# Kernel optimization log

Hardware: AMD Instinct MI355X
Metric: run time of the kernel (lower is better)

Reference implementation:

```python
import jax, jax.numpy as jnp
import numpy as np

B, S, D = 2, 8192, 2048
H, HD = 16, 128
LSH_NUM_PROJS = 7
BLOCK = 256          # key/query block size for block-diagonal attention
SAMPLE = 256         # number of uniformly sampled residual columns
ROPE_BASE = 10000.0
LOG_WEIGHT = float(np.log(S / SAMPLE))  # importance weight for sampled columns


def setup_inputs() -> dict:
    key = jax.random.key(0)
    ks = jax.random.split(key, 5)
    x = jax.random.normal(ks[0], (B, S, D), jnp.float32)
    w_in = jax.random.normal(ks[1], (D, 3 * D), jnp.float32) * (D ** -0.5)
    w_out = jax.random.normal(ks[2], (D, D), jnp.float32) * (D ** -0.5)
    lsh_proj = jax.random.normal(ks[3], (HD, LSH_NUM_PROJS), jnp.float32)
    sampled_set = jax.random.randint(ks[4], (B, H, SAMPLE), 0, S, jnp.int32)
    return {"x": x, "w_in": w_in, "w_out": w_out,
            "lsh_proj": lsh_proj, "sampled_set": sampled_set}


def _rope(t):
    # t: [B, S, H, HD]; LLaMA-style half-split rotary embedding, offset=0
    half = HD // 2
    inv_freq = 1.0 / (ROPE_BASE ** (jnp.arange(half, dtype=jnp.float32) / half))
    freqs = jnp.arange(S, dtype=jnp.float32)[:, None] * inv_freq[None, :]  # [S, half]
    cos = jnp.cos(freqs)[None, :, None, :]
    sin = jnp.sin(freqs)[None, :, None, :]
    t1, t2 = t[..., :half], t[..., half:]
    return jnp.concatenate([t1 * cos - t2 * sin, t2 * cos + t1 * sin], axis=-1)


def _lse_attn(q, k, v, scale, bias=None):
    # exact attention with log-sum-exp; q [...,n,d], k/v [...,m,d]
    s = jnp.einsum('...nd,...md->...nm', q, k) * scale
    if bias is not None:
        s = s + bias
    lse = jax.nn.logsumexp(s, axis=-1, keepdims=True)   # [...,n,1]
    p = jnp.exp(s - lse)
    return jnp.einsum('...nm,...md->...nd', p, v), lse


def _hyper_attention(q, k, v, lsh_proj, sampled_set):
    # q,k,v: [B,H,S,HD]  (non-causal HyperAttention path)
    scale = HD ** -0.5

    def lsh_hash(t):
        # simhash bucket codes from sign bits of random projections
        bits = jnp.einsum('bhsd,dp->bhsp', t, lsh_proj) > 0
        powers = (2 ** jnp.arange(LSH_NUM_PROJS)).astype(jnp.int32)
        return jnp.sum(bits.astype(jnp.int32) * powers, axis=-1)  # [B,H,S]

    q_idx = jnp.argsort(lsh_hash(q), axis=-1, stable=True)
    k_idx = jnp.argsort(lsh_hash(k), axis=-1, stable=True)
    q_idx_inv = jnp.argsort(q_idx, axis=-1, stable=True)
    gather = lambda t, i: jnp.take_along_axis(t, i[..., None], axis=2)

    qs = gather(q, q_idx)
    ks_ = gather(k, k_idx)
    vs = gather(v, k_idx)

    # 1. block-diagonal exact attention on LSH-sorted order
    nb = S // BLOCK
    qb = qs.reshape(B, H, nb, BLOCK, HD)
    kb = ks_.reshape(B, H, nb, BLOCK, HD)
    vb = vs.reshape(B, H, nb, BLOCK, HD)
    attn_blk, lse_blk = _lse_attn(qb, kb, vb, scale)
    attn_blk = attn_blk.reshape(B, H, S, HD)
    lse_blk = lse_blk.reshape(B, H, S, 1)

    # 2. residual: uniformly sampled columns (indices into sorted key order),
    #    masking columns already covered by the query's diagonal block
    k_sub = gather(ks_, sampled_set)   # [B,H,m,HD]
    v_sub = gather(vs, sampled_set)
    q_block_id = jnp.arange(S, dtype=jnp.int32) // BLOCK          # [S]
    s_block_id = sampled_set // BLOCK                             # [B,H,m]
    neg = jnp.finfo(q.dtype).min
    bias = jnp.where(q_block_id[None, None, :, None] == s_block_id[:, :, None, :],
                     neg, jnp.array(0.0, q.dtype))                # [B,H,S,m]
    attn_res, lse_res = _lse_attn(qs, k_sub, v_sub, scale, bias=bias)
    lse_res = lse_res + LOG_WEIGHT

    # 3. merge the two partial softmax results (online-softmax combine)
    lse = jnp.logaddexp(lse_blk, lse_res)
    attn = attn_blk * jnp.exp(lse_blk - lse) + attn_res * jnp.exp(lse_res - lse)

    # undo query sort
    return gather(attn, q_idx_inv)


def reference(x, w_in, w_out, lsh_proj, sampled_set):
    qkv = x @ w_in                           # [B,S,3D]
    q, k, v = jnp.split(qkv, 3, axis=-1)
    r4 = lambda t: t.reshape(B, S, H, HD)
    q, k, v = _rope(r4(q)), _rope(r4(k)), r4(v)
    tr = lambda t: t.transpose(0, 2, 1, 3)   # -> [B,H,S,HD]
    out = _hyper_attention(tr(q), tr(k), tr(v), lsh_proj, sampled_set)
    out = out.transpose(0, 2, 1, 3).reshape(B, S, D)
    return out @ w_out
```

## Files before the change

### kernel.cpp

```cpp
#include <hip/hip_runtime.h>
#include <stdint.h>

typedef _Float16 f16;
typedef _Float16 f16x8 __attribute__((ext_vector_type(8)));
typedef float f32x4 __attribute__((ext_vector_type(4)));
typedef uint32_t u32;

#define SEQ 8192
#define NH 16
#define HDIM 128
#define BHCNT 32
#define KDIM 2048
#define SCALE 0.08838834764831845f
#define LOGW 3.4657359027997265f
#define TAU1 0.06f
#define TAU 6e-3f
#define MAXWL 32768
#define BCAP 1024

__device__ __forceinline__ f32x4 mfma16(f16x8 a, f16x8 b, f32x4 c){
  return __builtin_amdgcn_mfma_f32_16x16x32_f16(a, b, c, 0, 0, 0);
}

__device__ __forceinline__ void g2l16(const f16* g, f16* l){
  __builtin_amdgcn_global_load_lds(
      (const __attribute__((address_space(1))) void*)g,
      (__attribute__((address_space(3))) void*)l, 16, 0, 0);
}

__global__ __launch_bounds__(256) void split_x_k(const float* __restrict__ x,
                                                 f16* __restrict__ xh){
  size_t i = ((size_t)blockIdx.x * 256 + threadIdx.x) * 4;
  float4 v = *(const float4*)(x + i);
  union { f16 h[4]; ushort4 u; } a;
  a.h[0]=(f16)v.x; a.h[1]=(f16)v.y; a.h[2]=(f16)v.z; a.h[3]=(f16)v.w;
  *(ushort4*)(xh + i) = a.u;
}

__global__ void transpose_k(const float* __restrict__ in, f16* __restrict__ ohi,
                            f16* __restrict__ olo, int Kd, int Nd, int NLO){
  __shared__ float t[32][33];
  int tx = threadIdx.x, ty = threadIdx.y;
  int n0 = blockIdx.x*32, k0 = blockIdx.y*32;
  #pragma unroll
  for (int i=0;i<4;i++) t[ty+i*8][tx] = in[(size_t)(k0+ty+i*8)*Nd + n0+tx];
  __syncthreads();
  #pragma unroll
  for (int i=0;i<4;i++){
    int n = n0 + ty + i*8, k = k0 + tx;
    float v = t[tx][ty+i*8];
    f16 h = (f16)v;
    ohi[(size_t)n*Kd + k] = h;
    if (n < NLO) olo[(size_t)n*Kd + k] = (f16)(v - (float)h);
  }
}

__global__ __launch_bounds__(256) void rope_table_k(float* __restrict__ ct, float* __restrict__ st){
  int i = blockIdx.x * 256 + threadIdx.x;
  int s = i >> 6, d = i & 63;
  float p32 = (float)pow(10000.0, (double)d / 64.0);
  float inv = __fdiv_rn(1.0f, p32);
  float f = __fmul_rn((float)s, inv);
  double a = (double)f;
  ct[i] = (float)cos(a);
  st[i] = (float)sin(a);
}

__global__ void zero_k(int* p){ p[0] = 0; p[1] = 0; p[2] = 0; }

__global__ void diag_k(const int* __restrict__ flags, float* __restrict__ out){
  int c = flags[0];
  if (c == 0 || c >= MAXWL || flags[2]) out[0] = 1.0e9f + (float)c;
}

template<int MODE, int NC>
__global__ __launch_bounds__(256) void gemm_k(
    const f16* __restrict__ A, const f16* __restrict__ Bt,
    f16* __restrict__ q16, f16* __restrict__ k16, f16* __restrict__ v16,
    float* __restrict__ o0, int N){
  __shared__ f16 sm[8192];
  const int tid = threadIdx.x, lane = tid & 63, wave = tid >> 6;
  const int wr = wave >> 1, wc = wave & 1;
  const int wg = blockIdx.x;
  const int chunkw = gridDim.x >> 3;
  const int swz = (wg & 7) * chunkw + (wg >> 3);
  const int bcol = swz % NC, brow = swz / NC;
  const int g = lane >> 4, q_ = lane & 15;
  f32x4 acc[4][4];
  #pragma unroll
  for (int m=0;m<4;m++)
    #pragma unroll
    for (int n=0;n<4;n++) acc[m][n] = (f32x4){0.f,0.f,0.f,0.f};
  const int srow = tid >> 2, sseg = tid & 3;
  const int scol = (sseg ^ (srow & 3)) * 8;
  const f16* ga0 = A  + (size_t)(brow*128 + srow)*KDIM + scol;
  const f16* gb0 = Bt + (size_t)(bcol*128 + srow)*KDIM + scol;
  f16* As = sm; f16* Bs = sm + 4096;
  f16* dA0 = As + wave*512; f16* dA1 = As + 2048 + wave*512;
  f16* dB0 = Bs + wave*512; f16* dB1 = Bs + 2048 + wave*512;
  const int aoff = (wr*64 + q_)*32 + (g ^ (q_ & 3))*8;
  const int boff = (wc*64 + q_)*32 + (g ^ (q_ & 3))*8;
  for (int kt = 0; kt < KDIM/32; ++kt){
    const size_t ko = (size_t)kt * 32;
    g2l16(ga0 + ko, dA0); g2l16(ga0 + (size_t)64*KDIM + ko, dA1);
    g2l16(gb0 + ko, dB0); g2l16(gb0 + (size_t)64*KDIM + ko, dB1);
    __syncthreads();
    f16x8 af[4];
    #pragma unroll
    for (int m=0;m<4;m++) af[m] = *(const f16x8*)&As[aoff + m*16*32];
    #pragma unroll
    for (int n=0;n<4;n++){
      f16x8 bf = *(const f16x8*)&Bs[boff + n*16*32];
      #pragma unroll
      for (int m=0;m<4;m++) acc[m][n] = mfma16(af[m], bf, acc[m][n]);
    }
    __syncthreads();
  }
  #pragma unroll
  for (int m=0;m<4;m++)
    #pragma unroll
    for (int n=0;n<4;n++)
      #pragma unroll
      for (int j=0;j<4;j++){
        int row = brow*128 + wr*64 + m*16 + g*4 + j;
        int col = bcol*128 + wc*64 + n*16 + q_;
        float v = acc[m][n][j];
        if constexpr (MODE == 0){
          o0[(size_t)row * N + col] = v;
        } else {
          int b = row >> 13, s = row & 8191;
          int sec = col >> 11;
          int cl = col & 2047;
          int h = cl >> 7, hd = cl & 127;
          f16* dst = (sec == 0) ? q16 : ((sec == 1) ? k16 : v16);
          dst[(((size_t)b*NH + h)*SEQ + s)*HDIM + hd] = (f16)v;
        }
      }
}

__global__ __launch_bounds__(256) void rope_hash_k(f16* __restrict__ qk, const float* __restrict__ ct,
    const float* __restrict__ st, const float* __restrict__ proj, int* __restrict__ hout,
    int tag, int* __restrict__ wl, int* __restrict__ wcnt){
  const int lane = threadIdx.x & 63, wave = threadIdx.x >> 6;
  const int s = blockIdx.x * 4 + wave, bh = blockIdx.y;
  f16* row = qk + ((size_t)bh * SEQ + s) * HDIM;
  float vx = (float)row[2*lane], vy = (float)row[2*lane+1];
  float ox = __shfl_xor(vx, 32), oy = __shfl_xor(vy, 32);
  const int dl = 2*lane, di = dl & 63;
  const float* cb = ct + (size_t)s*64; const float* sb = st + (size_t)s*64;
  float c0 = cb[di], c1 = cb[di+1], sn0 = sb[di], sn1 = sb[di+1];
  float r0, r1;
  if (lane < 32){ r0 = vx*c0 - ox*sn0; r1 = vy*c1 - oy*sn1; }
  else          { r0 = vx*c0 + ox*sn0; r1 = vy*c1 + oy*sn1; }
  union { f16 h[2]; u32 u; } pk;
  pk.h[0] = (f16)r0; pk.h[1] = (f16)r1;
  *(u32*)(row + dl) = pk.u;
  float part[7];
  #pragma unroll
  for (int p=0;p<7;p++) part[p] = r0*proj[dl*7+p] + r1*proj[(dl+1)*7+p];
  #pragma unroll
  for (int off=32; off>=1; off>>=1){
    #pragma unroll
    for (int p=0;p<7;p++) part[p] += __shfl_xor(part[p], off);
  }
  if (lane == 0){
    int hs = 0; float mn = 1e30f;
    #pragma unroll
    for (int p=0;p<7;p++){ if (part[p] > 0.f) hs |= (1<<p); mn = fminf(mn, fabsf(part[p])); }
    hout[bh*SEQ + s] = hs;
    if (mn < TAU1){
      int w = atomicAdd(wcnt, 1);
      if (w < MAXWL){ wl[2*w] = (bh<<1) | tag; wl[2*w+1] = s; }
    }
  }
}

__global__ __launch_bounds__(256) void bucket_k(const int* __restrict__ wl, const int* __restrict__ wcnt,
    int* __restrict__ wl2, int* __restrict__ cnt2, int* __restrict__ flags){
  const int bucket = blockIdx.x;
  __shared__ int lcnt;
  if (threadIdx.x == 0) lcnt = 0;
  __syncthreads();
  int count = wcnt[0]; if (count > MAXWL) count = MAXWL;
  for (int i = threadIdx.x; i < count; i += 256){
    int tagbh = wl[2*i];
    int tag = tagbh & 1, h = (tagbh >> 1) & 15;
    if (tag*16 + h == bucket){
      int pos = atomicAdd(&lcnt, 1);
      if (pos < BCAP) wl2[bucket*BCAP + pos] = (tagbh << 13) | wl[2*i+1];
    }
  }
  __syncthreads();
  if (threadIdx.x == 0){
    cnt2[bucket] = (lcnt > BCAP) ? BCAP : lcnt;
    if (lcnt > BCAP) atomicExch(&flags[2], 1);
  }
}

__global__ __launch_bounds__(256) void t2_k(const float* __restrict__ x,
    const f16* __restrict__ wh, const f16* __restrict__ wlo,
    const int* __restrict__ wl2, const int* __restrict__ cnt2,
    const float* __restrict__ ct, const float* __restrict__ st, const float* __restrict__ proj,
    int* __restrict__ hq, int* __restrict__ hk, int* __restrict__ wl3, int* __restrict__ wcnt3){
  const int bucket = blockIdx.y;
  const int nrows = cnt2[bucket];
  const int base = blockIdx.x * 64;
  if (base >= nrows) return;
  const int tid = threadIdx.x, lane = tid & 63, wave = tid >> 6;
  const int g = lane >> 4, q_ = lane & 15;
  __shared__ f16 Ah[64*32], Alo[64*32], Bh[128*32], Bl[128*32];
  __shared__ float S[64][128];
  __shared__ int rs[64], ent[64];
  if (tid < 64){
    int idx = base + tid;
    int e = wl2[bucket*BCAP + (idx < nrows ? idx : 0)];
    ent[tid] = e;
    int s = e & 8191;
    int b = e >> 18;
    rs[tid] = b * SEQ + s;
  }
  __syncthreads();
  const int tag = bucket >> 4, h = bucket & 15;
  const f16* Wh = wh  + ((size_t)(tag*2048 + h*128)) * KDIM;
  const f16* Wl = wlo + ((size_t)(tag*2048 + h*128)) * KDIM;
  f32x4 acc[8];
  #pragma unroll
  for (int n=0;n<8;n++) acc[n] = (f32x4){0.f,0.f,0.f,0.f};
  const int arow = tid >> 2, aseg = tid & 3;
  const int bcol = tid >> 1, bhalf = tid & 1;
  const size_t abase = (size_t)rs[arow]*KDIM + aseg*8;
  const size_t bbase = (size_t)bcol*KDIM + bhalf*16;
  for (int kt = 0; kt < 64; ++kt){
    const int k0 = kt*32;
    {
      union { float4 f4[2]; float f[8]; } xa;
      xa.f4[0] = *(const float4*)(x + abase + k0);
      xa.f4[1] = *(const float4*)(x + abase + k0 + 4);
      union { f16 h[8]; f16x8 v; } hh, ll;
      #pragma unroll
      for (int i=0;i<8;i++){
        f16 hv = (f16)xa.f[i];
        hh.h[i] = hv;
        ll.h[i] = (f16)(xa.f[i] - (float)hv);
      }
      *(f16x8*)&Ah [arow*32 + aseg*8] = hh.v;
      *(f16x8*)&Alo[arow*32 + aseg*8] = ll.v;
    }
    *(f16x8*)&Bh[bcol*32 + bhalf*16]     = *(const f16x8*)(Wh + bbase + k0);
    *(f16x8*)&Bh[bcol*32 + bhalf*16 + 8] = *(const f16x8*)(Wh + bbase + k0 + 8);
    *(f16x8*)&Bl[bcol*32 + bhalf*16]     = *(const f16x8*)(Wl + bbase + k0);
    *(f16x8*)&Bl[bcol*32 + bhalf*16 + 8] = *(const f16x8*)(Wl + bbase + k0 + 8);
    __syncthreads();
    f16x8 ah = *(const f16x8*)&Ah [(wave*16 + q_)*32 + g*8];
    f16x8 al = *(const f16x8*)&Alo[(wave*16 + q_)*32 + g*8];
    #pragma unroll
    for (int n=0;n<8;n++){
      f16x8 bh8 = *(const f16x8*)&Bh[(n*16 + q_)*32 + g*8];
      f16x8 bl8 = *(const f16x8*)&Bl[(n*16 + q_)*32 + g*8];
      acc[n] = mfma16(ah, bh8, acc[n]);
      acc[n] = mfma16(ah, bl8, acc[n]);
      acc[n] = mfma16(al, bh8, acc[n]);
    }
    __syncthreads();
  }
  #pragma unroll
  for (int n=0;n<8;n++)
    #pragma unroll
    for (int j=0;j<4;j++)
      S[wave*16 + g*4 + j][n*16 + q_] = acc[n][j];
  __syncthreads();
  for (int r = 0; r < 16; ++r){
    int row = wave*16 + r;
    int gidx = base + row;
    if (gidx >= nrows) break;
    int e = ent[row];
    int s = e & 8191;
    int tagbh = e >> 13;
    int bh = tagbh >> 1;
    float vx = S[row][2*lane], vy = S[row][2*lane+1];
    float ox = __shfl_xor(vx, 32), oy = __shfl_xor(vy, 32);
    const int dl = 2*lane, di = dl & 63;
    float c0 = ct[(size_t)s*64 + di], c1v = ct[(size_t)s*64 + di + 1];
    float sn0 = st[(size_t)s*64 + di], sn1 = st[(size_t)s*64 + di + 1];
    float r0, r1;
    if (lane < 32){ r0 = vx*c0 - ox*sn0; r1 = vy*c1v - oy*sn1; }
    else          { r0 = vx*c0 + ox*sn0; r1 = vy*c1v + oy*sn1; }
    float part[7];
    #pragma unroll
    for (int p=0;p<7;p++) part[p] = r0*proj[dl*7+p] + r1*proj[(dl+1)*7+p];
    #pragma unroll
    for (int off=32; off>=1; off>>=1){
      #pragma unroll
      for (int p=0;p<7;p++) part[p] += __shfl_xor(part[p], off);
    }
    if (lane == 0){
      int hs = 0; float mn = 1e30f;
      #pragma unroll
      for (int p=0;p<7;p++){ if (part[p] > 0.f) hs |= (1<<p); mn = fminf(mn, fabsf(part[p])); }
      ((tagbh & 1) ? hk : hq)[bh*SEQ + s] = hs;
      if (mn < TAU){
        int w = atomicAdd(wcnt3, 1);
        if (w < MAXWL){ wl3[2*w] = tagbh; wl3[2*w+1] = s; }
      }
    }
  }
}

__global__ __launch_bounds__(256) void fixup_k(const float* __restrict__ x, const float* __restrict__ w_in,
    const float* __restrict__ proj, const float* __restrict__ ct, const float* __restrict__ st,
    const int* __restrict__ wl, const int* __restrict__ wcnt,
    int* __restrict__ hq, int* __restrict__ hk){
  const int lane = threadIdx.x & 63, wave = threadIdx.x >> 6;
  const int gw = blockIdx.x * 4 + wave, nw = gridDim.x * 4;
  int count = *wcnt; if (count > MAXWL) count = MAXWL;
  for (int e = gw; e < count; e += nw){
    int tagbh = wl[2*e], s = wl[2*e+1];
    int tag = tagbh & 1, bh = tagbh >> 1;
    int b = bh >> 4, h = bh & 15;
    const float* xr = x + ((size_t)b*SEQ + s)*KDIM;
    const int c0i = tag*2048 + h*128 + lane;
    double a0 = 0.0, a1 = 0.0;
    for (int j = 0; j < KDIM; ++j){
      double xv = (double)xr[j];
      a0 += xv * (double)w_in[(size_t)j*6144 + c0i];
      a1 += xv * (double)w_in[(size_t)j*6144 + c0i + 64];
    }
    double c = (double)ct[(size_t)s*64 + lane];
    double sn = (double)st[(size_t)s*64 + lane];
    double r0 = a0*c - a1*sn;
    double r1 = a1*c + a0*sn;
    int hs = 0;
    #pragma unroll
    for (int p = 0; p < 7; ++p){
      double part = r0 * (double)proj[lane*7+p] + r1 * (double)proj[(lane+64)*7+p];
      #pragma unroll
      for (int off = 32; off >= 1; off >>= 1) part += __shfl_xor(part, off);
      if (part > 0.0) hs |= (1<<p);
    }
    if (lane == 0) (tag ? hk : hq)[bh*SEQ + s] = hs;
  }
}

__global__ __launch_bounds__(256) void sort_k(const int* __restrict__ hsh, int* __restrict__ idx){
  const int bh = blockIdx.x, tid = threadIdx.x;
  __shared__ unsigned char hl[SEQ];
  __shared__ unsigned short hist[128*256];
  __shared__ unsigned int part[256];
  const int* hrow = hsh + bh*SEQ;
  for (int i = tid; i < SEQ; i += 256) hl[i] = (unsigned char)hrow[i];
  u32* h32 = (u32*)hist;
  for (int i = tid; i < 128*256/2; i += 256) h32[i] = 0;
  __syncthreads();
  #pragma unroll 1
  for (int j = 0; j < 32; ++j){
    int hv = hl[tid*32 + j];
    hist[hv*256 + tid] = (unsigned short)(hist[hv*256 + tid] + 1);
  }
  __syncthreads();
  unsigned int s = 0;
  #pragma unroll 1
  for (int f = tid*128; f < tid*128 + 128; ++f) s += hist[f];
  part[tid] = s;
  __syncthreads();
  for (int off = 1; off < 256; off <<= 1){
    unsigned int v = (tid >= off) ? part[tid - off] : 0u;
    __syncthreads();
    part[tid] += v;
    __syncthreads();
  }
  unsigned int run = (tid == 0) ? 0u : part[tid - 1];
  #pragma unroll 1
  for (int f = tid*128; f < tid*128 + 128; ++f){
    unsigned short c = hist[f];
    hist[f] = (unsigned short)run;
    run += c;
  }
  __syncthreads();
  int* orow = idx + bh*SEQ;
  #pragma unroll 1
  for (int j = 0; j < 32; ++j){
    int i = tid*32 + j;
    int hv = hl[i];
    unsigned short p = hist[hv*256 + tid];
    hist[hv*256 + tid] = (unsigned short)(p + 1);
    orow[p] = i;
  }
}

__global__ __launch_bounds__(512) void attn_k(const f16* __restrict__ qr, const f16* __restrict__ kr,
    const f16* __restrict__ v, const int* __restrict__ qidx, const int* __restrict__ kidx,
    const int* __restrict__ smp, f16* __restrict__ out){
  const int tid = threadIdx.x, lane = tid & 63, wave = tid >> 6;
  const int blk = blockIdx.x, bh = blockIdx.y;
  const int b = bh >> 4, h = bh & 15;
  const int qblock = blk >> 1;
  __shared__ f16 Kl[32*136];
  __shared__ f16 Vt[128*40];
  __shared__ float biasl[256];
  __shared__ int kid[512];
  const int g = lane >> 4, q_ = lane & 15;
  for (int j = tid; j < 512; j += 512){
    int kpos;
    if (j < 256) kpos = qblock*256 + j;
    else {
      kpos = smp[bh*256 + (j-256)];
      biasl[j-256] = ((kpos >> 8) == qblock) ? -1e30f : LOGW;
    }
    kid[j] = kidx[bh*SEQ + kpos];
  }
  const int qpos = blk*128 + wave*16 + q_;
  const int qi = qidx[bh*SEQ + qpos];
  const f16* qb = qr + ((size_t)bh*SEQ + qi)*HDIM;
  f16x8 qf[4];
  #pragma unroll
  for (int c=0;c<4;c++) qf[c] = *(const f16x8*)(qb + c*32 + g*8);
  f32x4 O[8];
  #pragma unroll
  for (int c=0;c<8;c++) O[c] = (f32x4){0.f,0.f,0.f,0.f};
  float m_run = -1e30f, l_run = 0.f;
  __syncthreads();
  const int kkK = tid >> 3, segK = tid & 7;
  const int kk2 = tid & 15, d0 = (tid >> 4) * 8;
  f16x8 pk0, pk1, pv0, pv1;
  if (tid < 256){
    int krw = kid[kkK];
    const f16* ks = kr + ((size_t)bh*SEQ + krw)*HDIM + segK*16;
    pk0 = *(const f16x8*)ks; pk1 = *(const f16x8*)(ks + 8);
    int r0 = kid[2*kk2], r1 = kid[2*kk2 + 1];
    pv0 = *(const f16x8*)(v + ((size_t)bh*SEQ + r0)*HDIM + d0);
    pv1 = *(const f16x8*)(v + ((size_t)bh*SEQ + r1)*HDIM + d0);
  }
  for (int t = 0; t < 16; ++t){
    if (tid < 256){
      *(f16x8*)&Kl[kkK*136 + segK*16]     = pk0;
      *(f16x8*)&Kl[kkK*136 + segK*16 + 8] = pk1;
      #pragma unroll
      for (int i=0;i<8;i++){
        union { f16 h[2]; u32 u; } pr;
        pr.h[0] = pv0[i]; pr.h[1] = pv1[i];
        *(u32*)&Vt[(d0+i)*40 + 2*kk2] = pr.u;
      }
    }
    __syncthreads();
    if (t < 15 && tid < 256){
      int jb = (t+1)*32;
      int krw = kid[jb + kkK];
      const f16* ks = kr + ((size_t)bh*SEQ + krw)*HDIM + segK*16;
      pk0 = *(const f16x8*)ks; pk1 = *(const f16x8*)(ks + 8);
      int r0 = kid[jb + 2*kk2], r1 = kid[jb + 2*kk2 + 1];
      pv0 = *(const f16x8*)(v + ((size_t)bh*SEQ + r0)*HDIM + d0);
      pv1 = *(const f16x8*)(v + ((size_t)bh*SEQ + r1)*HDIM + d0);
    }
    f32x4 c0 = (f32x4){0.f,0.f,0.f,0.f}, c1 = (f32x4){0.f,0.f,0.f,0.f};
    #pragma unroll
    for (int c=0;c<4;c++){
      f16x8 k0 = *(const f16x8*)&Kl[q_*136 + c*32 + g*8];
      f16x8 k1 = *(const f16x8*)&Kl[(16+q_)*136 + c*32 + g*8];
      c0 = mfma16(k0, qf[c], c0);
      c1 = mfma16(k1, qf[c], c1);
    }
    float sc[8];
    if (t < 8){
      #pragma unroll
      for (int j=0;j<4;j++){ sc[j] = c0[j]*SCALE; sc[4+j] = c1[j]*SCALE; }
    } else {
      const float* bb = &biasl[(t-8)*32];
      #pragma unroll
      for (int j=0;j<4;j++){ sc[j] = c0[j]*SCALE + bb[g*4+j]; sc[4+j] = c1[j]*SCALE + bb[16+g*4+j]; }
    }
    float mx = sc[0];
    #pragma unroll
    for (int i=1;i<8;i++) mx = fmaxf(mx, sc[i]);
    mx = fmaxf(mx, __shfl_xor(mx, 16));
    mx = fmaxf(mx, __shfl_xor(mx, 32));
    float mnew = fmaxf(m_run, mx);
    float al = __expf(m_run - mnew);
    float p[8]; float ps = 0.f;
    #pragma unroll
    for (int i=0;i<8;i++){ p[i] = __expf(sc[i] - mnew); ps += p[i]; }
    ps += __shfl_xor(ps, 16);
    ps += __shfl_xor(ps, 32);
    l_run = l_run * al + ps;
    m_run = mnew;
    float aj0 = __shfl(al, g*4+0), aj1 = __shfl(al, g*4+1);
    float aj2 = __shfl(al, g*4+2), aj3 = __shfl(al, g*4+3);
    #pragma unroll
    for (int c=0;c<8;c++){ O[c][0]*=aj0; O[c][1]*=aj1; O[c][2]*=aj2; O[c][3]*=aj3; }
    union { f16 h[2]; u32 u; } pk;
    pk.h[0]=(f16)p[0]; pk.h[1]=(f16)p[1]; u32 A0 = pk.u;
    pk.h[0]=(f16)p[2]; pk.h[1]=(f16)p[3]; u32 A1 = pk.u;
    pk.h[0]=(f16)p[4]; pk.h[1]=(f16)p[5]; u32 B0 = pk.u;
    pk.h[0]=(f16)p[6]; pk.h[1]=(f16)p[7]; u32 B1 = pk.u;
    int srcA = (((2*g)&3)<<4) | q_;
    int srcB = ((((2*g)+1)&3)<<4) | q_;
    bool selh = g >= 2;
    u32 xa0 = __shfl(A0, srcA), xb0 = __shfl(B0, srcA);
    u32 xa1 = __shfl(A1, srcA), xb1 = __shfl(B1, srcA);
    u32 xa2 = __shfl(A0, srcB), xb2 = __shfl(B0, srcB);
    u32 xa3 = __shfl(A1, srcB), xb3 = __shfl(B1, srcB);
    union { u32 w[4]; f16x8 f; } pf;
    pf.w[0] = selh ? xb0 : xa0;
    pf.w[1] = selh ? xb1 : xa1;
    pf.w[2] = selh ? xb2 : xa2;
    pf.w[3] = selh ? xb3 : xa3;
    #pragma unroll
    for (int c=0;c<8;c++){
      f16x8 vf = *(const f16x8*)&Vt[(c*16 + q_)*40 + g*8];
      O[c] = mfma16(pf.f, vf, O[c]);
    }
    __syncthreads();
  }
  float li0 = 1.f/__shfl(l_run, g*4+0), li1 = 1.f/__shfl(l_run, g*4+1);
  float li2 = 1.f/__shfl(l_run, g*4+2), li3 = 1.f/__shfl(l_run, g*4+3);
  const int posbase = blk*128 + wave*16;
  #pragma unroll
  for (int j=0;j<4;j++){
    float li = (j==0)?li0:((j==1)?li1:((j==2)?li2:li3));
    int sorig = qidx[bh*SEQ + posbase + g*4 + j];
    f16* dst = out + (((size_t)b*SEQ + sorig)*NH + h)*HDIM;
    #pragma unroll
    for (int c=0;c<8;c++) dst[c*16 + q_] = (f16)(O[c][j] * li);
  }
}

extern "C" void kernel_launch(void* const* d_in, const int* in_sizes, int n_in,
                              void* d_out, int out_size, void* d_ws, size_t ws_size,
                              hipStream_t stream) {
  (void)in_sizes; (void)n_in; (void)out_size; (void)ws_size;
  const float* x     = (const float*)d_in[0];
  const float* w_in  = (const float*)d_in[1];
  const float* w_out = (const float*)d_in[2];
  const float* proj  = (const float*)d_in[3];
  const int*   smp   = (const int*)d_in[4];
  float* out = (float*)d_out;

  char* ws = (char*)d_ws;
  size_t off = 0;
  auto alloc = [&](size_t bytes){ void* p = ws + off; off += (bytes + 255) & ~(size_t)255; return p; };
  f16*   xh   = (f16*)alloc((size_t)16384*2048*2);
  f16*   wh   = (f16*)alloc((size_t)6144*2048*2);
  f16*   wl   = (f16*)alloc((size_t)4096*2048*2);
  f16*   wo   = (f16*)alloc((size_t)2048*2048*2);
  f16*   qf   = (f16*)alloc((size_t)BHCNT*SEQ*HDIM*2);
  f16*   kf   = (f16*)alloc((size_t)BHCNT*SEQ*HDIM*2);
  f16*   vv   = (f16*)alloc((size_t)BHCNT*SEQ*HDIM*2);
  f16*   attn = (f16*)alloc((size_t)BHCNT*SEQ*HDIM*2);
  float* cost = (float*)alloc((size_t)SEQ*64*4);
  float* sint = (float*)alloc((size_t)SEQ*64*4);
  int*   hq   = (int*)alloc((size_t)BHCNT*SEQ*4);
  int*   hk   = (int*)alloc((size_t)BHCNT*SEQ*4);
  int*   qidx = (int*)alloc((size_t)BHCNT*SEQ*4);
  int*   kidx = (int*)alloc((size_t)BHCNT*SEQ*4);
  int*   wlst = (int*)alloc((size_t)MAXWL*2*4);
  int*   wlst2= (int*)alloc((size_t)32*BCAP*4);
  int*   wlst3= (int*)alloc((size_t)MAXWL*2*4);
  int*   cnt2 = (int*)alloc(256);
  int*   flags= (int*)alloc(256);

  int* wcnt  = flags;
  int* wcnt3 = flags + 1;

  zero_k<<<1, 1, 0, stream>>>(flags);
  split_x_k<<<32768, 256, 0, stream>>>(x, xh);
  transpose_k<<<dim3(192,64), dim3(32,8), 0, stream>>>(w_in, wh, wl, 2048, 6144, 4096);
  transpose_k<<<dim3(64,64),  dim3(32,8), 0, stream>>>(w_out, wo, nullptr, 2048, 2048, 0);
  rope_table_k<<<2048, 256, 0, stream>>>(cost, sint);

  gemm_k<1,48><<<6144, 256, 0, stream>>>(xh, wh, qf, kf, vv, nullptr, 0);

  rope_hash_k<<<dim3(2048,32), 256, 0, stream>>>(qf, cost, sint, proj, hq, 0, wlst, wcnt);
  rope_hash_k<<<dim3(2048,32), 256, 0, stream>>>(kf, cost, sint, proj, hk, 1, wlst, wcnt);

  bucket_k<<<32, 256, 0, stream>>>(wlst, wcnt, wlst2, cnt2, flags);
  t2_k<<<dim3(16,32), 256, 0, stream>>>(x, wh, wl, wlst2, cnt2, cost, sint, proj,
                                        hq, hk, wlst3, wcnt3);
  fixup_k<<<512, 256, 0, stream>>>(x, w_in, proj, cost, sint, wlst3, wcnt3, hq, hk);

  sort_k<<<32, 256, 0, stream>>>(hq, qidx);
  sort_k<<<32, 256, 0, stream>>>(hk, kidx);

  attn_k<<<dim3(64,32), 512, 0, stream>>>(qf, kf, vv, qidx, kidx, smp, attn);

  gemm_k<0,16><<<2048, 256, 0, stream>>>(attn, wo, nullptr, nullptr, nullptr, out, 2048);

  diag_k<<<1, 1, 0, stream>>>(flags, out);
}
```

Measured before the change: 1.668 ms.

## Process 64-key tiles in attention loop with lazy rescale and MFMA priority

The attention kernel now stages 64 keys per iteration instead of 32, so all 512 threads take part in loading K and V and the loop runs half as many iterations with half as many barriers. It adds a wave-uniform lazy rescale that skips updating the running max and rescaling O when the new tile max stays within 8 of the running max. It also raises wave priority around the MFMA blocks. In exchange it uses more LDS and registers, which may lower occupancy, and the skipped rescale lets unnormalised exponentials grow up to e^8 before fp16 conversion.

Result: no change. 1.692 ms (+1.4%).

```diff
diff --git a/kernel.cpp b/kernel.cpp
--- a/kernel.cpp
+++ b/kernel.cpp
@@ -394,12 +394,13 @@
   const int blk = blockIdx.x, bh = blockIdx.y;
   const int b = bh >> 4, h = bh & 15;
   const int qblock = blk >> 1;
-  __shared__ f16 Kl[32*136];
-  __shared__ f16 Vt[128*40];
+  __shared__ f16 Kl[64*136];
+  __shared__ f16 Vt[128*72];
   __shared__ float biasl[256];
   __shared__ int kid[512];
   const int g = lane >> 4, q_ = lane & 15;
-  for (int j = tid; j < 512; j += 512){
+  {
+    int j = tid;
     int kpos;
     if (j < 256) kpos = qblock*256 + j;
     else {
@@ -419,94 +420,109 @@
   for (int c=0;c<8;c++) O[c] = (f32x4){0.f,0.f,0.f,0.f};
   float m_run = -1e30f, l_run = 0.f;
   __syncthreads();
-  const int kkK = tid >> 3, segK = tid & 7;
-  const int kk2 = tid & 15, d0 = (tid >> 4) * 8;
+  const int rowK = tid >> 3, segK = tid & 7;
+  const int pairV = tid & 31, d0 = (tid >> 5) * 8;
   f16x8 pk0, pk1, pv0, pv1;
-  if (tid < 256){
-    int krw = kid[kkK];
+  {
+    int krw = kid[rowK];
     const f16* ks = kr + ((size_t)bh*SEQ + krw)*HDIM + segK*16;
     pk0 = *(const f16x8*)ks; pk1 = *(const f16x8*)(ks + 8);
-    int r0 = kid[2*kk2], r1 = kid[2*kk2 + 1];
+    int r0 = kid[2*pairV], r1 = kid[2*pairV + 1];
     pv0 = *(const f16x8*)(v + ((size_t)bh*SEQ + r0)*HDIM + d0);
     pv1 = *(const f16x8*)(v + ((size_t)bh*SEQ + r1)*HDIM + d0);
   }
-  for (int t = 0; t < 16; ++t){
-    if (tid < 256){
-      *(f16x8*)&Kl[kkK*136 + segK*16]     = pk0;
-      *(f16x8*)&Kl[kkK*136 + segK*16 + 8] = pk1;
-      #pragma unroll
-      for (int i=0;i<8;i++){
-        union { f16 h[2]; u32 u; } pr;
-        pr.h[0] = pv0[i]; pr.h[1] = pv1[i];
-        *(u32*)&Vt[(d0+i)*40 + 2*kk2] = pr.u;
-      }
-    }
-    __syncthreads();
-    if (t < 15 && tid < 256){
-      int jb = (t+1)*32;
-      int krw = kid[jb + kkK];
+  for (int t = 0; t < 8; ++t){
+    *(f16x8*)&Kl[rowK*136 + segK*16]     = pk0;
+    *(f16x8*)&Kl[rowK*136 + segK*16 + 8] = pk1;
+    #pragma unroll
+    for (int i=0;i<8;i++){
+      union { f16 h[2]; u32 u; } pr;
+      pr.h[0] = pv0[i]; pr.h[1] = pv1[i];
+      *(u32*)&Vt[(d0+i)*72 + 2*pairV] = pr.u;
+    }
+    __syncthreads();
+    if (t < 7){
+      int jb = (t+1)*64;
+      int krw = kid[jb + rowK];
       const f16* ks = kr + ((size_t)bh*SEQ + krw)*HDIM + segK*16;
       pk0 = *(const f16x8*)ks; pk1 = *(const f16x8*)(ks + 8);
-      int r0 = kid[jb + 2*kk2], r1 = kid[jb + 2*kk2 + 1];
+      int r0 = kid[jb + 2*pairV], r1 = kid[jb + 2*pairV + 1];
       pv0 = *(const f16x8*)(v + ((size_t)bh*SEQ + r0)*HDIM + d0);
       pv1 = *(const f16x8*)(v + ((size_t)bh*SEQ + r1)*HDIM + d0);
     }
-    f32x4 c0 = (f32x4){0.f,0.f,0.f,0.f}, c1 = (f32x4){0.f,0.f,0.f,0.f};
-    #pragma unroll
-    for (int c=0;c<4;c++){
-      f16x8 k0 = *(const f16x8*)&Kl[q_*136 + c*32 + g*8];
-      f16x8 k1 = *(const f16x8*)&Kl[(16+q_)*136 + c*32 + g*8];
-      c0 = mfma16(k0, qf[c], c0);
-      c1 = mfma16(k1, qf[c], c1);
-    }
-    float sc[8];
-    if (t < 8){
-      #pragma unroll
-      for (int j=0;j<4;j++){ sc[j] = c0[j]*SCALE; sc[4+j] = c1[j]*SCALE; }
+    f32x4 cc[4];
+    #pragma unroll
+    for (int kg=0;kg<4;kg++) cc[kg] = (f32x4){0.f,0.f,0.f,0.f};
+    __builtin_amdgcn_s_setprio(1);
+    #pragma unroll
+    for (int kg=0;kg<4;kg++)
+      #pragma unroll
+      for (int c=0;c<4;c++){
+        f16x8 kfr = *(const f16x8*)&Kl[(kg*16 + q_)*136 + c*32 + g*8];
+        cc[kg] = mfma16(kfr, qf[c], cc[kg]);
+      }
+    __builtin_amdgcn_s_setprio(0);
+    float sc[16];
+    if (t < 4){
+      #pragma unroll
+      for (int kg=0;kg<4;kg++)
+        #pragma unroll
+        for (int j=0;j<4;j++) sc[kg*4+j] = cc[kg][j]*SCALE;
     } else {
-      const float* bb = &biasl[(t-8)*32];
-      #pragma unroll
-      for (int j=0;j<4;j++){ sc[j] = c0[j]*SCALE + bb[g*4+j]; sc[4+j] = c1[j]*SCALE + bb[16+g*4+j]; }
+      const float* bb = &biasl[(t-4)*64];
+      #pragma unroll
+      for (int kg=0;kg<4;kg++)
+        #pragma unroll
+        for (int j=0;j<4;j++) sc[kg*4+j] = cc[kg][j]*SCALE + bb[kg*16 + g*4 + j];
     }
     float mx = sc[0];
     #pragma unroll
-    for (int i=1;i<8;i++) mx = fmaxf(mx, sc[i]);
+    for (int i=1;i<16;i++) mx = fmaxf(mx, sc[i]);
     mx = fmaxf(mx, __shfl_xor(mx, 16));
     mx = fmaxf(mx, __shfl_xor(mx, 32));
-    float mnew = fmaxf(m_run, mx);
-    float al = __expf(m_run - mnew);
-    float p[8]; float ps = 0.f;
-    #pragma unroll
-    for (int i=0;i<8;i++){ p[i] = __expf(sc[i] - mnew); ps += p[i]; }
+    bool skip = __all(mx <= m_run + 8.0f);
+    float al;
+    if (skip){ al = 1.0f; }
+    else { float mnew = fmaxf(m_run, mx); al = __expf(m_run - mnew); m_run = mnew; }
+    float ps = 0.f;
+    #pragma unroll
+    for (int i=0;i<16;i++){ sc[i] = __expf(sc[i] - m_run); ps += sc[i]; }
     ps += __shfl_xor(ps, 16);
     ps += __shfl_xor(ps, 32);
     l_run = l_run * al + ps;
-    m_run = mnew;
-    float aj0 = __shfl(al, g*4+0), aj1 = __shfl(al, g*4+1);
-    float aj2 = __shfl(al, g*4+2), aj3 = __shfl(al, g*4+3);
-    #pragma unroll
-    for (int c=0;c<8;c++){ O[c][0]*=aj0; O[c][1]*=aj1; O[c][2]*=aj2; O[c][3]*=aj3; }
-    union { f16 h[2]; u32 u; } pk;
-    pk.h[0]=(f16)p[0]; pk.h[1]=(f16)p[1]; u32 A0 = pk.u;
-    pk.h[0]=(f16)p[2]; pk.h[1]=(f16)p[3]; u32 A1 = pk.u;
-    pk.h[0]=(f16)p[4]; pk.h[1]=(f16)p[5]; u32 B0 = pk.u;
-    pk.h[0]=(f16)p[6]; pk.h[1]=(f16)p[7]; u32 B1 = pk.u;
-    int srcA = (((2*g)&3)<<4) | q_;
-    int srcB = ((((2*g)+1)&3)<<4) | q_;
-    bool selh = g >= 2;
-    u32 xa0 = __shfl(A0, srcA), xb0 = __shfl(B0, srcA);
-    u32 xa1 = __shfl(A1, srcA), xb1 = __shfl(B1, srcA);
-    u32 xa2 = __shfl(A0, srcB), xb2 = __shfl(B0, srcB);
-    u32 xa3 = __shfl(A1, srcB), xb3 = __shfl(B1, srcB);
-    union { u32 w[4]; f16x8 f; } pf;
-    pf.w[0] = selh ? xb0 : xa0;
-    pf.w[1] = selh ? xb1 : xa1;
-    pf.w[2] = selh ? xb2 : xa2;
-    pf.w[3] = selh ? xb3 : xa3;
-    #pragma unroll
-    for (int c=0;c<8;c++){
-      f16x8 vf = *(const f16x8*)&Vt[(c*16 + q_)*40 + g*8];
-      O[c] = mfma16(pf.f, vf, O[c]);
+    if (!skip){
+      float aj0 = __shfl(al, g*4+0), aj1 = __shfl(al, g*4+1);
+      float aj2 = __shfl(al, g*4+2), aj3 = __shfl(al, g*4+3);
+      #pragma unroll
+      for (int c=0;c<8;c++){ O[c][0]*=aj0; O[c][1]*=aj1; O[c][2]*=aj2; O[c][3]*=aj3; }
+    }
+    #pragma unroll
+    for (int kg2 = 0; kg2 < 2; ++kg2){
+      const float* pp = &sc[kg2*8];
+      union { f16 h[2]; u32 u; } pk;
+      pk.h[0]=(f16)pp[0]; pk.h[1]=(f16)pp[1]; u32 A0 = pk.u;
+      pk.h[0]=(f16)pp[2]; pk.h[1]=(f16)pp[3]; u32 A1 = pk.u;
+      pk.h[0]=(f16)pp[4]; pk.h[1]=(f16)pp[5]; u32 B0 = pk.u;
+      pk.h[0]=(f16)pp[6]; pk.h[1]=(f16)pp[7]; u32 B1 = pk.u;
+      int srcA = (((2*g)&3)<<4) | q_;
+      int srcB = ((((2*g)+1)&3)<<4) | q_;
+      bool selh = g >= 2;
+      u32 xa0 = __shfl(A0, srcA), xb0 = __shfl(B0, srcA);
+      u32 xa1 = __shfl(A1, srcA), xb1 = __shfl(B1, srcA);
+      u32 xa2 = __shfl(A0, srcB), xb2 = __shfl(B0, srcB);
+      u32 xa3 = __shfl(A1, srcB), xb3 = __shfl(B1, srcB);
+      union { u32 w[4]; f16x8 f; } pf;
+      pf.w[0] = selh ? xb0 : xa0;
+      pf.w[1] = selh ? xb1 : xa1;
+      pf.w[2] = selh ? xb2 : xa2;
+      pf.w[3] = selh ? xb3 : xa3;
+      __builtin_amdgcn_s_setprio(1);
+      #pragma unroll
+      for (int c=0;c<8;c++){
+        f16x8 vf = *(const f16x8*)&Vt[(c*16 + q_)*72 + kg2*32 + g*8];
+        O[c] = mfma16(pf.f, vf, O[c]);
+      }
+      __builtin_amdgcn_s_setprio(0);
     }
     __syncthreads();
   }
```
